# Kernel tuning notes

Hardware: AMD Instinct MI355X
Metric: run time of the kernel (lower is better)

Reference implementation:

```python
import jax, jax.numpy as jnp
import numpy as np

B, L, D = 8, 2048, 512


def setup_inputs() -> dict:
    key = jax.random.key(0)
    ks = jax.random.split(key, 6)
    s = 0.02
    return {
        "q": jax.random.normal(ks[0], (B, L, D), jnp.float32),
        "k": jax.random.normal(ks[1], (B, L, D), jnp.float32),
        "v": jax.random.normal(ks[2], (B, L, D), jnp.float32),
        "Wq": jax.random.normal(ks[3], (D, D), jnp.float32) * s,
        "bq": jnp.zeros((D,), jnp.float32),
        "Wk": jax.random.normal(ks[4], (D, D), jnp.float32) * s,
        "bk": jnp.zeros((D,), jnp.float32),
        "Wv": jax.random.normal(ks[5], (D, D), jnp.float32) * s,
        "bv": jnp.zeros((D,), jnp.float32),
    }


def reference(q, k, v, Wq, bq, Wk, bk, Wv, bv):
    # Linear projections (torch Linear: x @ W.T + b)
    qp = jnp.einsum("bld,ed->ble", q, Wq) + bq
    kp = jnp.einsum("bld,ed->ble", k, Wk) + bk
    vp = jnp.einsum("bld,ed->ble", v, Wv) + bv
    # attn[b, i, j] = qp[b, i] . kp[b, j]   (no 1/sqrt(d) scaling in source)
    attn = jnp.einsum("bqd,bkd->bqk", qp, kp)
    # Faithful to torch.nn.Softmax(dim=1): normalize over the QUERY axis.
    attn = jax.nn.softmax(attn, axis=1)
    out = jnp.einsum("bqk,bkd->bqd", attn, vp)
    return out
```

## Files before the change

### kernel.cpp

```cpp
#include <hip/hip_runtime.h>
#include <math.h>


#define TKK 32

typedef __attribute__((ext_vector_type(8))) short bf16x8;
typedef __attribute__((ext_vector_type(4))) float floatx4;

typedef __attribute__((address_space(3))) short lds_short;
typedef const __attribute__((address_space(1))) short glob_short;

__device__ __forceinline__ short f2bf(float x) {
    unsigned u = __float_as_uint(x);
    u += 0x7fff + ((u >> 16) & 1);
    return (short)(u >> 16);
}
__device__ __forceinline__ float bf2f(short s) {
    return __uint_as_float(((unsigned)(unsigned short)s) << 16);
}

__global__ __launch_bounds__(256) void cast3_f32_bf16(
    const float* __restrict__ a, const float* __restrict__ b,
    const float* __restrict__ c,
    short* __restrict__ oa, short* __restrict__ ob, short* __restrict__ oc,
    long long n)
{
    const int z = blockIdx.y;
    const float* in  = (z == 0) ? a  : (z == 1) ? b  : c;
    short*       out = (z == 0) ? oa : (z == 1) ? ob : oc;
    long long i = ((long long)blockIdx.x * 256 + threadIdx.x) * 8;
    if (i + 8 > n) return;
    float4 x = *(const float4*)(in + i);
    float4 y = *(const float4*)(in + i + 4);
    bf16x8 r;
    r[0] = f2bf(x.x); r[1] = f2bf(x.y); r[2] = f2bf(x.z); r[3] = f2bf(x.w);
    r[4] = f2bf(y.x); r[5] = f2bf(y.y); r[6] = f2bf(y.z); r[7] = f2bf(y.w);
    *(bf16x8*)(out + i) = r;
}

__global__ __launch_bounds__(256) void zero_f32(float* __restrict__ p, int n)
{
    int i = blockIdx.x * 256 + threadIdx.x;
    if (i < n) p[i] = 0.f;
}

template<int TMp, int TNp, int WM, int WN, int HAS_BIAS, int OUT_BF16>
__device__ __forceinline__ void gemm_body(
    const short* __restrict__ A, const short* __restrict__ B,
    const float* __restrict__ bias, void* __restrict__ C,
    int N, int K, int m0, int n0)
{
    __shared__ short As[TMp * TKK];
    __shared__ short Bs[TNp * TKK];
    constexpr int MI = TMp / (16 * WM);
    constexpr int NJ = TNp / (16 * WN);
    const int t    = threadIdx.x;
    const int wave = t >> 6;
    const int lane = t & 63;
    const int wm = (wave / WN) * (TMp / WM);
    const int wn = (wave % WN) * (TNp / WN);
    const int sr = lane >> 2;
    const int sc = (lane & 3) * 8;

    floatx4 acc[MI][NJ];
    #pragma unroll
    for (int i = 0; i < MI; ++i)
        #pragma unroll
        for (int j = 0; j < NJ; ++j)
            acc[i][j] = (floatx4){0.f, 0.f, 0.f, 0.f};

    for (int k0 = 0; k0 < K; k0 += TKK) {
        #pragma unroll
        for (int c = wave; c < TMp / 16; c += 4)
            __builtin_amdgcn_global_load_lds(
                (glob_short*)(A + (long long)(m0 + c * 16 + sr) * K + k0 + sc),
                (lds_short*)(As + c * 512), 16, 0, 0);
        #pragma unroll
        for (int c = wave; c < TNp / 16; c += 4)
            __builtin_amdgcn_global_load_lds(
                (glob_short*)(B + (long long)(n0 + c * 16 + sr) * K + k0 + sc),
                (lds_short*)(Bs + c * 512), 16, 0, 0);
        __syncthreads();
        bf16x8 af[MI], bfr[NJ];
        #pragma unroll
        for (int i = 0; i < MI; ++i)
            af[i] = *(const bf16x8*)&As[(wm + i * 16 + (lane & 15)) * TKK + (lane >> 4) * 8];
        #pragma unroll
        for (int j = 0; j < NJ; ++j)
            bfr[j] = *(const bf16x8*)&Bs[(wn + j * 16 + (lane & 15)) * TKK + (lane >> 4) * 8];
        #pragma unroll
        for (int i = 0; i < MI; ++i)
            #pragma unroll
            for (int j = 0; j < NJ; ++j)
                acc[i][j] = __builtin_amdgcn_mfma_f32_16x16x32_bf16(af[i], bfr[j], acc[i][j], 0, 0, 0);
        __syncthreads();
    }

    #pragma unroll
    for (int i = 0; i < MI; ++i) {
        const int rbase = m0 + wm + i * 16 + (lane >> 4) * 4;
        #pragma unroll
        for (int j = 0; j < NJ; ++j) {
            const int col = n0 + wn + j * 16 + (lane & 15);
            const float bb = HAS_BIAS ? bias[col] : 0.f;
            #pragma unroll
            for (int r = 0; r < 4; ++r) {
                const long long off = (long long)(rbase + r) * N + col;
                const float vvv = acc[i][j][r] + bb;
                if (OUT_BF16) ((short*)C)[off] = f2bf(vvv);
                else          ((float*)C)[off] = vvv;
            }
        }
    }
}

__global__ __launch_bounds__(256) void proj_gemm(
    const short* __restrict__ x0, const short* __restrict__ x1, const short* __restrict__ x2,
    const short* __restrict__ w0, const short* __restrict__ w1, const short* __restrict__ w2,
    const float* __restrict__ b0, const float* __restrict__ b1, const float* __restrict__ b2,
    short* __restrict__ y0, short* __restrict__ y1, short* __restrict__ y2,
    int N, int K)
{
    const int z = blockIdx.z;
    const short* A    = (z == 0) ? x0 : (z == 1) ? x1 : x2;
    const short* B    = (z == 0) ? w0 : (z == 1) ? w1 : w2;
    const float* bias = (z == 0) ? b0 : (z == 1) ? b1 : b2;
    short*       C    = (z == 0) ? y0 : (z == 1) ? y1 : y2;
    gemm_body<128, 128, 2, 2, 1, 1>(A, B, bias, C, N, K,
                                    blockIdx.x * 128, blockIdx.y * 128);
}

__global__ __launch_bounds__(256) void pv_gemm(
    const short* __restrict__ E, const short* __restrict__ vpT,
    float* __restrict__ out, int N, int K,
    long long sA, long long sB, long long sC)
{
    const int bz = blockIdx.z;
    gemm_body<64, 128, 1, 4, 0, 0>(E + (long long)bz * sA, vpT + (long long)bz * sB,
                                   nullptr, out + (long long)bz * sC, N, K,
                                   blockIdx.x * 64, blockIdx.y * 128);
}

__global__ __launch_bounds__(256) void gemm_nt_exp_colsum(
    const short* __restrict__ A, const short* __restrict__ B,
    short* __restrict__ E, float* __restrict__ colsum,
    int N, int K, long long sA, long long sB, long long sE)
{
    __shared__ short As[128 * TKK];
    __shared__ short Bs[128 * TKK];
    __shared__ float wsum[4][64];
    const int bz = blockIdx.z;
    A += (long long)bz * sA;
    B += (long long)bz * sB;
    E += (long long)bz * sE;
    colsum += (long long)bz * N;

    const int m0 = blockIdx.x * 128;
    const int n0 = blockIdx.y * 128;
    const int t    = threadIdx.x;
    const int wave = t >> 6;
    const int lane = t & 63;
    const int wm = (wave >> 1) * 64;
    const int wn = (wave & 1)  * 64;
    const int sr = lane >> 2;
    const int sc = (lane & 3) * 8;

    floatx4 acc[4][4];
    #pragma unroll
    for (int i = 0; i < 4; ++i)
        #pragma unroll
        for (int j = 0; j < 4; ++j)
            acc[i][j] = (floatx4){0.f, 0.f, 0.f, 0.f};

    for (int k0 = 0; k0 < K; k0 += TKK) {
        #pragma unroll
        for (int it = 0; it < 2; ++it) {
            const int chunk = it * 4 + wave;
            const int r = chunk * 16 + sr;
            __builtin_amdgcn_global_load_lds(
                (glob_short*)(A + (long long)(m0 + r) * K + k0 + sc),
                (lds_short*)(As + chunk * 512), 16, 0, 0);
            __builtin_amdgcn_global_load_lds(
                (glob_short*)(B + (long long)(n0 + r) * K + k0 + sc),
                (lds_short*)(Bs + chunk * 512), 16, 0, 0);
        }
        __syncthreads();
        bf16x8 af[4], bfr[4];
        #pragma unroll
        for (int i = 0; i < 4; ++i)
            af[i] = *(const bf16x8*)&As[(wm + i * 16 + (lane & 15)) * TKK + (lane >> 4) * 8];
        #pragma unroll
        for (int j = 0; j < 4; ++j)
            bfr[j] = *(const bf16x8*)&Bs[(wn + j * 16 + (lane & 15)) * TKK + (lane >> 4) * 8];
        #pragma unroll
        for (int i = 0; i < 4; ++i)
            #pragma unroll
            for (int j = 0; j < 4; ++j)
                acc[i][j] = __builtin_amdgcn_mfma_f32_16x16x32_bf16(af[i], bfr[j], acc[i][j], 0, 0, 0);
        __syncthreads();
    }

    float csum[4] = {0.f, 0.f, 0.f, 0.f};
    #pragma unroll
    for (int i = 0; i < 4; ++i) {
        const int rbase = wm + i * 16 + (lane >> 4) * 4;
        #pragma unroll
        for (int j = 0; j < 4; ++j) {
            const int col = wn + j * 16 + (lane & 15);
            #pragma unroll
            for (int r = 0; r < 4; ++r) {
                const float e = __expf(acc[i][j][r]);
                E[(long long)(m0 + rbase + r) * N + (n0 + col)] = f2bf(e);
                csum[j] += e;
            }
        }
    }
    #pragma unroll
    for (int j = 0; j < 4; ++j) {
        csum[j] += __shfl_xor(csum[j], 16);
        csum[j] += __shfl_xor(csum[j], 32);
    }
    if (lane < 16) {
        #pragma unroll
        for (int j = 0; j < 4; ++j)
            wsum[wave][j * 16 + lane] = csum[j];
    }
    __syncthreads();
    if (t < 128) {
        const float s = (t < 64) ? (wsum[0][t] + wsum[2][t])
                                 : (wsum[1][t - 64] + wsum[3][t - 64]);
        atomicAdd(&colsum[n0 + t], s);
    }
}

__global__ __launch_bounds__(256) void transpose_scale_bf16(
    const short* __restrict__ in, const float* __restrict__ colsum,
    short* __restrict__ out, int R, int Cc)
{
    __shared__ short tile[32][33];
    const int b = blockIdx.z;
    in  += (long long)b * R * Cc;
    out += (long long)b * R * Cc;
    colsum += (long long)b * R;
    const int c0 = blockIdx.x * 32, r0 = blockIdx.y * 32;
    const int tx = threadIdx.x & 31, ty = threadIdx.x >> 5;
    #pragma unroll
    for (int rr = ty; rr < 32; rr += 8) {
        const float rs = 1.f / colsum[r0 + rr];
        tile[rr][tx] = f2bf(bf2f(in[(long long)(r0 + rr) * Cc + c0 + tx]) * rs);
    }
    __syncthreads();
    #pragma unroll
    for (int rr = ty; rr < 32; rr += 8)
        out[(long long)(c0 + rr) * R + r0 + tx] = tile[tx][rr];
}

extern "C" void kernel_launch(void* const* d_in, const int* in_sizes, int n_in,
                              void* d_out, int out_size, void* d_ws, size_t ws_size,
                              hipStream_t stream) {
    const float* q  = (const float*)d_in[0];
    const float* k  = (const float*)d_in[1];
    const float* v  = (const float*)d_in[2];
    const float* Wq = (const float*)d_in[3];
    const float* bq = (const float*)d_in[4];
    const float* Wk = (const float*)d_in[5];
    const float* bk = (const float*)d_in[6];
    const float* Wv = (const float*)d_in[7];
    const float* bv = (const float*)d_in[8];
    float* out = (float*)d_out;

    const int Bb = 8, L = 2048, D = 512;
    const long long BLD = (long long)Bb * L * D;
    const long long BLL = (long long)Bb * L * L;
    const long long DD  = (long long)D * D;

    short* base  = (short*)d_ws;
    short* q_bf  = base;
    short* k_bf  = q_bf  + BLD;
    short* v_bf  = k_bf  + BLD;
    short* qp_bf = v_bf  + BLD;
    short* kp_bf = qp_bf + BLD;
    short* vp_bf = kp_bf + BLD;
    short* vpT   = vp_bf + BLD;
    short* Wq_bf = vpT   + BLD;
    short* Wk_bf = Wq_bf + DD;
    short* Wv_bf = Wk_bf + DD;
    short* E_bf  = Wv_bf + DD;
    float* colsum = (float*)(E_bf + BLL);

    dim3 blk(256);

    cast3_f32_bf16<<<dim3(BLD / 2048, 3), blk, 0, stream>>>(
        q, k, v, q_bf, k_bf, v_bf, BLD);
    cast3_f32_bf16<<<dim3(DD / 2048, 3), blk, 0, stream>>>(
        Wq, Wk, Wv, Wq_bf, Wk_bf, Wv_bf, DD);
    zero_f32<<<dim3((Bb * L) / 256), blk, 0, stream>>>(colsum, Bb * L);

    dim3 gproj((Bb * L) / 128, D / 128, 3);
    proj_gemm<<<gproj, blk, 0, stream>>>(q_bf, k_bf, v_bf,
                                         Wq_bf, Wk_bf, Wv_bf,
                                         bq, bk, bv,
                                         qp_bf, kp_bf, vp_bf, D, D);

    dim3 gS(L / 128, L / 128, Bb);
    gemm_nt_exp_colsum<<<gS, blk, 0, stream>>>(qp_bf, kp_bf, E_bf, colsum,
                                               L, D,
                                               (long long)L * D, (long long)L * D,
                                               (long long)L * L);

    dim3 gT(D / 32, L / 32, Bb);
    transpose_scale_bf16<<<gT, blk, 0, stream>>>(vp_bf, colsum, vpT, L, D);

    dim3 gO(L / 64, D / 128, Bb);
    pv_gemm<<<gO, blk, 0, stream>>>(E_bf, vpT, out, D, L,
                                    (long long)L * L, (long long)D * L,
                                    (long long)L * D);
}
```

Baseline: 322.1 us.

## Fuse cast and zero kernels into one prep launch; retile PV GEMM to 64x64

```diff
diff --git a/kernel.cpp b/kernel.cpp
--- a/kernel.cpp
+++ b/kernel.cpp
@@ -19,29 +19,39 @@
     return __uint_as_float(((unsigned)(unsigned short)s) << 16);
 }
 
-__global__ __launch_bounds__(256) void cast3_f32_bf16(
-    const float* __restrict__ a, const float* __restrict__ b,
-    const float* __restrict__ c,
-    short* __restrict__ oa, short* __restrict__ ob, short* __restrict__ oc,
-    long long n)
-{
-    const int z = blockIdx.y;
-    const float* in  = (z == 0) ? a  : (z == 1) ? b  : c;
-    short*       out = (z == 0) ? oa : (z == 1) ? ob : oc;
-    long long i = ((long long)blockIdx.x * 256 + threadIdx.x) * 8;
-    if (i + 8 > n) return;
+__global__ __launch_bounds__(256) void prep(
+    const float* __restrict__ q, const float* __restrict__ k,
+    const float* __restrict__ v,
+    const float* __restrict__ Wq, const float* __restrict__ Wk,
+    const float* __restrict__ Wv,
+    short* __restrict__ q_bf, short* __restrict__ k_bf, short* __restrict__ v_bf,
+    short* __restrict__ Wq_bf, short* __restrict__ Wk_bf, short* __restrict__ Wv_bf,
+    float* __restrict__ colsum)
+{
+    const int b = blockIdx.x;
+    const float* in = nullptr;
+    short* out = nullptr;
+    long long i;
+    if (b < 12288) {
+        const int z = b >> 12;
+        in  = (z == 0) ? q    : (z == 1) ? k    : v;
+        out = (z == 0) ? q_bf : (z == 1) ? k_bf : v_bf;
+        i = ((long long)(b & 4095) * 256 + threadIdx.x) * 8;
+    } else if (b < 12672) {
+        const int z = (b - 12288) >> 7;
+        in  = (z == 0) ? Wq    : (z == 1) ? Wk    : Wv;
+        out = (z == 0) ? Wq_bf : (z == 1) ? Wk_bf : Wv_bf;
+        i = ((long long)((b - 12288) & 127) * 256 + threadIdx.x) * 8;
+    } else {
+        colsum[(b - 12672) * 256 + threadIdx.x] = 0.f;
+        return;
+    }
     float4 x = *(const float4*)(in + i);
     float4 y = *(const float4*)(in + i + 4);
     bf16x8 r;
     r[0] = f2bf(x.x); r[1] = f2bf(x.y); r[2] = f2bf(x.z); r[3] = f2bf(x.w);
     r[4] = f2bf(y.x); r[5] = f2bf(y.y); r[6] = f2bf(y.z); r[7] = f2bf(y.w);
     *(bf16x8*)(out + i) = r;
-}
-
-__global__ __launch_bounds__(256) void zero_f32(float* __restrict__ p, int n)
-{
-    int i = blockIdx.x * 256 + threadIdx.x;
-    if (i < n) p[i] = 0.f;
 }
 
 template<int TMp, int TNp, int WM, int WN, int HAS_BIAS, int OUT_BF16>
@@ -131,14 +141,75 @@
 }
 
 __global__ __launch_bounds__(256) void pv_gemm(
-    const short* __restrict__ E, const short* __restrict__ vpT,
-    float* __restrict__ out, int N, int K,
+    const short* __restrict__ Eg, const short* __restrict__ vpTg,
+    float* __restrict__ outg, int N, int K,
     long long sA, long long sB, long long sC)
 {
+    __shared__ short As[2][64 * TKK];
+    __shared__ short Bs[2][64 * TKK];
     const int bz = blockIdx.z;
-    gemm_body<64, 128, 1, 4, 0, 0>(E + (long long)bz * sA, vpT + (long long)bz * sB,
-                                   nullptr, out + (long long)bz * sC, N, K,
-                                   blockIdx.x * 64, blockIdx.y * 128);
+    const short* A = Eg   + (long long)bz * sA;
+    const short* B = vpTg + (long long)bz * sB;
+    float*       C = outg + (long long)bz * sC;
+
+    const int m0 = blockIdx.x * 64;
+    const int n0 = blockIdx.y * 64;
+    const int t    = threadIdx.x;
+    const int wave = t >> 6;
+    const int lane = t & 63;
+    const int wm = (wave >> 1) * 32;
+    const int wn = (wave & 1)  * 32;
+    const int sr = lane >> 2;
+    const int sc = (lane & 3) * 8;
+
+    floatx4 acc[2][2];
+    #pragma unroll
+    for (int i = 0; i < 2; ++i)
+        #pragma unroll
+        for (int j = 0; j < 2; ++j)
+            acc[i][j] = (floatx4){0.f, 0.f, 0.f, 0.f};
+
+    for (int k0 = 0; k0 < K; k0 += 2 * TKK) {
+        #pragma unroll
+        for (int h = 0; h < 2; ++h) {
+            const int kk = k0 + h * TKK;
+            __builtin_amdgcn_global_load_lds(
+                (glob_short*)(A + (long long)(m0 + wave * 16 + sr) * K + kk + sc),
+                (lds_short*)(As[h] + wave * 512), 16, 0, 0);
+            __builtin_amdgcn_global_load_lds(
+                (glob_short*)(B + (long long)(n0 + wave * 16 + sr) * K + kk + sc),
+                (lds_short*)(Bs[h] + wave * 512), 16, 0, 0);
+        }
+        __syncthreads();
+        #pragma unroll
+        for (int h = 0; h < 2; ++h) {
+            bf16x8 af[2], bfr[2];
+            #pragma unroll
+            for (int i = 0; i < 2; ++i)
+                af[i] = *(const bf16x8*)&As[h][(wm + i * 16 + (lane & 15)) * TKK + (lane >> 4) * 8];
+            #pragma unroll
+            for (int j = 0; j < 2; ++j)
+                bfr[j] = *(const bf16x8*)&Bs[h][(wn + j * 16 + (lane & 15)) * TKK + (lane >> 4) * 8];
+            #pragma unroll
+            for (int i = 0; i < 2; ++i)
+                #pragma unroll
+                for (int j = 0; j < 2; ++j)
+                    acc[i][j] = __builtin_amdgcn_mfma_f32_16x16x32_bf16(af[i], bfr[j], acc[i][j], 0, 0, 0);
+        }
+        __syncthreads();
+    }
+
+    #pragma unroll
+    for (int i = 0; i < 2; ++i) {
+        const int rbase = m0 + wm + i * 16 + (lane >> 4) * 4;
+        #pragma unroll
+        for (int j = 0; j < 2; ++j) {
+            const int col = n0 + wn + j * 16 + (lane & 15);
+            #pragma unroll
+            for (int r = 0; r < 4; ++r)
+                C[(long long)(rbase + r) * N + col] = acc[i][j][r];
+        }
+    }
 }
 
 __global__ __launch_bounds__(256) void gemm_nt_exp_colsum(
@@ -290,11 +361,9 @@
 
     dim3 blk(256);
 
-    cast3_f32_bf16<<<dim3(BLD / 2048, 3), blk, 0, stream>>>(
-        q, k, v, q_bf, k_bf, v_bf, BLD);
-    cast3_f32_bf16<<<dim3(DD / 2048, 3), blk, 0, stream>>>(
-        Wq, Wk, Wv, Wq_bf, Wk_bf, Wv_bf, DD);
-    zero_f32<<<dim3((Bb * L) / 256), blk, 0, stream>>>(colsum, Bb * L);
+    prep<<<dim3(12736), blk, 0, stream>>>(q, k, v, Wq, Wk, Wv,
+                                          q_bf, k_bf, v_bf,
+                                          Wq_bf, Wk_bf, Wv_bf, colsum);
 
     dim3 gproj((Bb * L) / 128, D / 128, 3);
     proj_gemm<<<gproj, blk, 0, stream>>>(q_bf, k_bf, v_bf,
@@ -311,7 +380,7 @@
     dim3 gT(D / 32, L / 32, Bb);
     transpose_scale_bf16<<<gT, blk, 0, stream>>>(vp_bf, colsum, vpT, L, D);
 
-    dim3 gO(L / 64, D / 128, Bb);
+    dim3 gO(L / 64, D / 64, Bb);
     pv_gemm<<<gO, blk, 0, stream>>>(E_bf, vpT, out, D, L,
                                     (long long)L * L, (long long)D * L,
                                     (long long)L * D);
```

Result: faster. 312.4 us (-3.0%).
